# Kernel tuning notes

Measured on AMD Instinct MI355X. Metric: run time of the kernel, lower is better.

## Reference

```python
import jax, jax.numpy as jnp
import numpy as np

B, T, I, H, O = 256, 256, 16, 256, 11
HYP_HID = 512
BLD = 8
N1 = H * I + H * H + 2 * H        # RNN cell params (W_ih, W_hh, b_ih, b_hh)
N2 = O * H + O                    # readout params (W_out, b_out)


def setup_inputs() -> dict:
    key = jax.random.key(0)
    k = jax.random.split(key, 4)
    bld = jax.random.normal(k[0], (B, BLD), dtype=jnp.float32)
    stimulus = jax.random.normal(k[1], (B, T, I), dtype=jnp.float32)
    # hypnet MLP: bld -> relu -> flat per-sample params; small init to keep tanh unsaturated
    W1 = jax.random.normal(k[2], (BLD, HYP_HID), dtype=jnp.float32) * 0.05
    b1 = jnp.zeros((HYP_HID,), dtype=jnp.float32)
    W2 = jax.random.normal(k[3], (HYP_HID, N1 + N2), dtype=jnp.float32) * 0.02
    b2 = jnp.zeros((N1 + N2,), dtype=jnp.float32)
    return {"bld": bld, "stimulus": stimulus, "W1": W1, "b1": b1, "W2": W2, "b2": b2}


def reference(bld, stimulus, W1, b1, W2, b2):
    # hypernetwork: per-sample flat params [B, N1+N2]
    flat = jax.nn.relu(bld @ W1 + b1) @ W2 + b2
    params1, params2 = flat[:, :N1], flat[:, N1:]

    # unpack per-sample RNN cell params
    o = 0
    W_ih = params1[:, o:o + H * I].reshape(B, H, I); o += H * I
    W_hh = params1[:, o:o + H * H].reshape(B, H, H); o += H * H
    b_ih = params1[:, o:o + H]; o += H
    b_hh = params1[:, o:o + H]
    W_out = params2[:, :O * H].reshape(B, O, H)
    b_out = params2[:, O * H:].reshape(B, O)

    # shift stimulus right by one step with a zero frame (teacher forcing input)
    rnn_input = jnp.concatenate(
        [jnp.zeros((B, 1, I), dtype=stimulus.dtype), stimulus[:, :-1]], axis=1)

    # precompute input projection for all steps: [B, T, H]
    x_proj = jnp.einsum('bti,bhi->bth', rnn_input, W_ih) + b_ih[:, None, :]

    def step(h, xp_t):  # h: [B, H], xp_t: [B, H]
        h_next = jnp.tanh(xp_t + jnp.einsum('bh,bgh->bg', h, W_hh) + b_hh)
        return h_next, h_next

    h0 = jnp.zeros((B, H), dtype=stimulus.dtype)
    h_last, out_tm = jax.lax.scan(step, h0, jnp.swapaxes(x_proj, 0, 1))
    output1 = jnp.swapaxes(out_tm, 0, 1)  # [B, T, H]

    # per-sample linear readout [B, T, O]
    output2 = jnp.einsum('bth,boh->bto', output1, W_out) + b_out[:, None, :]
    output2 = jnp.nan_to_num(output2, nan=0.0)

    output_act = jax.nn.sigmoid(output2[:, :, :3])
    output_bldi = output2[:, :, 3:]
    h = h_last[None]  # [1, B, H]
    return (output_act, output_bldi, h, params1, params2)
```

## Files before the change

kernel.cpp:

```cpp
#include <hip/hip_runtime.h>

typedef unsigned short u16;
typedef unsigned int u32;
using short8   = __attribute__((ext_vector_type(8))) short;
using floatx4  = __attribute__((ext_vector_type(4))) float;
using half_t   = _Float16;
using half2_t  = __attribute__((ext_vector_type(2))) _Float16;
using halfx8   = __attribute__((ext_vector_type(8))) _Float16;

constexpr int B_ = 256, T_ = 256, I_ = 16, H_ = 256, O_ = 11;
constexpr int HYP = 512;
constexpr int N1_ = H_ * I_ + H_ * H_ + 2 * H_;
constexpr int N2_ = O_ * H_ + O_;
constexpr int GN  = N1_ + N2_;

constexpr size_t OUT_ACT  = 0;
constexpr size_t OUT_BLDI = (size_t)B_ * T_ * 3;
constexpr size_t OUT_H    = OUT_BLDI + (size_t)B_ * T_ * 8;
constexpr size_t OUT_P1   = OUT_H + (size_t)B_ * H_;
constexpr size_t OUT_P2   = OUT_P1 + (size_t)B_ * N1_;

__device__ inline void bar_lds() {
    asm volatile("s_waitcnt lgkmcnt(0)\n\ts_barrier" ::: "memory");
}

__device__ inline float bf2f(u16 u) {
    union { u32 i; float f; } v; v.i = ((u32)u) << 16; return v.f;
}
__device__ inline u16 f2bf(float f) {
    u32 x = __float_as_uint(f);
    u32 r = (x + 0x7fffu + ((x >> 16) & 1u)) >> 16;
    return (u16)r;
}

__device__ inline bool sniff_f32(const void* p) {
    const u16* w = (const u16*)p;
    const int lane = threadIdx.x & 63;
    u16 u = w[lane * 2];
    unsigned e = (u >> 7) & 0xFF;
    bool inband = (u == 0) || (e >= 77 && e <= 140);
    return __popcll(__ballot(inband)) < 56;
}

__device__ inline float ldr(const void* p, size_t i, bool f32) {
    return f32 ? ((const float*)p)[i] : bf2f(((const u16*)p)[i]);
}

__global__ void h1_kernel(const void* __restrict__ bld, const void* __restrict__ W1,
                          const void* __restrict__ b1, u16* __restrict__ h1) {
    const bool bldf = sniff_f32(bld);
    const bool w1f  = sniff_f32(W1);
    const bool b1f  = sniff_f32(b1);
    const int b = blockIdx.x;
    const int j = threadIdx.x;
    float acc = ldr(b1, j, b1f);
#pragma unroll
    for (int k = 0; k < 8; k++)
        acc += ldr(bld, b * 8 + k, bldf) * ldr(W1, k * HYP + j, w1f);
    h1[b * HYP + j] = f2bf(fmaxf(acc, 0.f));
}

constexpr int KS_ = 32;
constexpr int NST = HYP / KS_;
constexpr int TKP = 40;

template<bool W2F32>
__device__ void gemm_body(const u16* __restrict__ A, const void* __restrict__ Bm,
                          const void* __restrict__ b2, bool b2f,
                          float* __restrict__ out) {
    __shared__ alignas(16) u16 tileT[64][TKP];

    const int nb   = blockIdx.x * 64;
    const int tid  = threadIdx.x;
    const int lane = tid & 63;
    const int wid  = tid >> 6;
    const int l15  = lane & 15;
    const int q    = lane >> 4;

    int  col[4]; bool cv[4];
#pragma unroll
    for (int j = 0; j < 4; j++) {
        int c = nb + j * 16 + l15;
        cv[j]  = (c < GN);
        col[j] = cv[j] ? c : (GN - 1);
    }

    const u16* ap[4];
#pragma unroll
    for (int i = 0; i < 4; i++)
        ap[i] = A + (wid * 64 + i * 16 + l15) * HYP + q * 8;

    const int scol_i = tid & 63;
    const int kq     = tid >> 6;
    int gc = nb + scol_i;
    if (gc >= GN) gc = GN - 1;
    const size_t colOff = (size_t)gc;

    float pf[8]; u16 pb[8];
    {
#pragma unroll
        for (int e = 0; e < 8; e++) {
            const size_t ro = (size_t)(kq * 8 + e) * (size_t)GN + colOff;
            if constexpr (W2F32) pf[e] = ((const float*)Bm)[ro];
            else                 pb[e] = ((const u16*)Bm)[ro];
        }
    }

    floatx4 acc[4][4] = {};

    for (int ks = 0; ks < NST; ks++) {
        short8 wv8;
#pragma unroll
        for (int e = 0; e < 8; e++) {
            if constexpr (W2F32) wv8[e] = (short)f2bf(pf[e]);
            else                 wv8[e] = (short)pb[e];
        }
        *(short8*)&tileT[scol_i][kq * 8] = wv8;

        if (ks + 1 < NST) {
#pragma unroll
            for (int e = 0; e < 8; e++) {
                const size_t ro = (size_t)((ks + 1) * KS_ + kq * 8 + e) * (size_t)GN + colOff;
                if constexpr (W2F32) pf[e] = ((const float*)Bm)[ro];
                else                 pb[e] = ((const u16*)Bm)[ro];
            }
        }
        bar_lds();

        short8 af[4];
#pragma unroll
        for (int i = 0; i < 4; i++)
            af[i] = *(const short8*)(ap[i] + ks * KS_);

        short8 bfr[4];
#pragma unroll
        for (int j = 0; j < 4; j++)
            bfr[j] = *(const short8*)&tileT[j * 16 + l15][q * 8];

#pragma unroll
        for (int i = 0; i < 4; i++)
#pragma unroll
            for (int j = 0; j < 4; j++)
                acc[i][j] = __builtin_amdgcn_mfma_f32_16x16x32_bf16(af[i], bfr[j], acc[i][j], 0, 0, 0);
        bar_lds();
    }

    const bool isP2 = (nb >= N1_);
#pragma unroll
    for (int j = 0; j < 4; j++) {
        const float bias = ldr(b2, col[j], b2f);
#pragma unroll
        for (int i = 0; i < 4; i++) {
            const int mbase = wid * 64 + i * 16 + q * 4;
#pragma unroll
            for (int r = 0; r < 4; r++) {
                if (cv[j]) {
                    const float v = acc[i][j][r] + bias;
                    const int m = mbase + r;
                    size_t dst;
                    if (isP2) dst = OUT_P2 + (size_t)m * N2_ + (size_t)(col[j] - N1_);
                    else      dst = OUT_P1 + (size_t)m * N1_ + (size_t)col[j];
                    out[dst] = v;
                }
            }
        }
    }
}
__global__ __launch_bounds__(256) void gemm_kernel(const u16* A, const void* Bm,
                                                   const void* b2, float* out) {
    const bool w2f = sniff_f32(Bm);
    const bool b2f = sniff_f32(b2);
    if (w2f) gemm_body<true>(A, Bm, b2, b2f, out);
    else     gemm_body<false>(A, Bm, b2, b2f, out);
}

constexpr int HROW = 256;
constexpr int XROW = 40;

__global__ __launch_bounds__(256, 1) void rnn_kernel(const void* __restrict__ stim,
                                                     float* __restrict__ out) {
    const bool stf = sniff_f32(stim);
    const int b    = blockIdx.x;
    const int tid  = threadIdx.x;
    const int lane = tid & 63;
    const int wv   = tid >> 6;
    const int l15  = lane & 15;
    const int q    = lane >> 4;

    const float* p1 = out + OUT_P1 + (size_t)b * N1_;
    const float* p2 = out + OUT_P2 + (size_t)b * N2_;

    __shared__ alignas(16) half_t hist[(T_ + 1) * HROW];
    __shared__ alignas(16) half_t stim_s[T_ * XROW];

    if (stf) {
        const float2* sp = (const float2*)stim + (size_t)b * T_ * 8;
        for (int idx = tid; idx < (T_ - 1) * 8; idx += 256) {
            const int tt = idx >> 3, pr = idx & 7;
            float2 v = sp[idx];
            half2_t h; h.x = (half_t)v.x; h.y = (half_t)v.y;
            *(half2_t*)&stim_s[(tt + 1) * XROW + pr * 2] = h;
        }
    } else {
        const u32* sp = (const u32*)((const u16*)stim + (size_t)b * T_ * I_);
        for (int idx = tid; idx < (T_ - 1) * 8; idx += 256) {
            const int tt = idx >> 3, pr = idx & 7;
            u32 u = sp[idx];
            union { u32 i; float f; } lo2, hi2;
            lo2.i = u << 16; hi2.i = u & 0xffff0000u;
            half2_t h; h.x = (half_t)lo2.f; h.y = (half_t)hi2.f;
            *(half2_t*)&stim_s[(tt + 1) * XROW + pr * 2] = h;
        }
    }
    {
        u32* ss = (u32*)stim_s;
        const int base = tid * (XROW / 2);
        ss[base + 8] = 0x00003C00u;
#pragma unroll
        for (int z = 9; z < XROW / 2; z++) ss[base + z] = 0u;
        if (tid < 8)   ss[tid] = 0u;
        if (tid < 128) ((u32*)hist)[tid] = 0u;
    }

    halfx8 Wf[4][9];
    {
        const float* WH  = p1 + H_ * I_;
        const float* BIH = p1 + H_ * I_ + H_ * H_;
#pragma unroll
        for (int i = 0; i < 4; i++) {
            const int rr = 64 * wv + i * 16 + l15;
#pragma unroll
            for (int kt = 0; kt < 8; kt++) {
                const float4* wp = (const float4*)(WH + (size_t)rr * H_ + kt * 32 + q * 8);
                float4 r0 = wp[0], r1 = wp[1];
                halfx8 f;
                f[0] = (half_t)r0.x; f[1] = (half_t)r0.y; f[2] = (half_t)r0.z; f[3] = (half_t)r0.w;
                f[4] = (half_t)r1.x; f[5] = (half_t)r1.y; f[6] = (half_t)r1.z; f[7] = (half_t)r1.w;
                Wf[i][kt] = f;
            }
            halfx8 fx;
#pragma unroll
            for (int j = 0; j < 8; j++) fx[j] = (half_t)0.f;
            if (q < 2) {
                const float4* ip = (const float4*)(p1 + (size_t)rr * I_ + q * 8);
                float4 r0 = ip[0], r1 = ip[1];
                fx[0] = (half_t)r0.x; fx[1] = (half_t)r0.y; fx[2] = (half_t)r0.z; fx[3] = (half_t)r0.w;
                fx[4] = (half_t)r1.x; fx[5] = (half_t)r1.y; fx[6] = (half_t)r1.z; fx[7] = (half_t)r1.w;
            } else if (q == 2) {
                fx[0] = (half_t)(BIH[rr] + BIH[H_ + rr]);
            }
            Wf[i][8] = fx;
        }
    }
    __syncthreads();

    for (int t = 0; t < T_; t++) {
        halfx8 af[9];
        const half_t* hr = hist + (size_t)t * HROW + q * 8;
#pragma unroll
        for (int kt = 0; kt < 8; kt++)
            af[kt] = *(const halfx8*)(hr + kt * 32);
        af[8] = *(const halfx8*)(stim_s + (size_t)t * XROW + q * 8);

        floatx4 acc[4] = {};
#pragma unroll
        for (int kt = 0; kt < 9; kt++)
#pragma unroll
            for (int i = 0; i < 4; i++)
                acc[i] = __builtin_amdgcn_mfma_f32_16x16x32_f16(af[kt], Wf[i][kt], acc[i], 0, 0, 0);

        half_t* hw = hist + (size_t)(t + 1) * HROW;
#pragma unroll
        for (int i = 0; i < 4; i++) {
            const float s  = acc[i][0];
            const float e  = __expf(2.f * s);
            const float hn = 1.f - 2.f / (e + 1.f);
            if (lane < 16) {
                hw[64 * wv + i * 16 + l15] = (half_t)hn;
                if (t == T_ - 1) out[OUT_H + (size_t)b * H_ + 64 * wv + i * 16 + l15] = hn;
            }
        }
        bar_lds();
    }

    halfx8 Wo[8];
    float bo = 0.f;
    {
#pragma unroll
        for (int kt = 0; kt < 8; kt++) {
            halfx8 f;
#pragma unroll
            for (int j = 0; j < 8; j++) f[j] = (half_t)0.f;
            if (l15 < O_) {
                const float* wp = p2 + (size_t)l15 * H_ + kt * 32 + q * 8;
#pragma unroll
                for (int j = 0; j < 8; j++) f[j] = (half_t)wp[j];
            }
            Wo[kt] = f;
        }
        if (l15 < O_) bo = p2[O_ * H_ + l15];
    }

#pragma unroll
    for (int m = 0; m < 4; m++) {
        const int tb = (4 * wv + m) * 16;
        const half_t* hr = hist + (size_t)(tb + l15 + 1) * HROW + q * 8;
        floatx4 acc = {};
#pragma unroll
        for (int kt = 0; kt < 8; kt++) {
            halfx8 a = *(const halfx8*)(hr + kt * 32);
            acc = __builtin_amdgcn_mfma_f32_16x16x32_f16(a, Wo[kt], acc, 0, 0, 0);
        }
        if (l15 < O_) {
            const int o = l15;
#pragma unroll
            for (int r = 0; r < 4; r++) {
                const int tt = tb + q * 4 + r;
                float v2 = acc[r] + bo;
                if (o < 3) out[OUT_ACT + (size_t)b * T_ * 3 + (size_t)tt * 3 + o] = 1.f / (1.f + __expf(-v2));
                else       out[OUT_BLDI + (size_t)b * T_ * 8 + (size_t)tt * 8 + (o - 3)] = v2;
            }
        }
    }
}

extern "C" void kernel_launch(void* const* d_in, const int* in_sizes, int n_in,
                              void* d_out, int out_size, void* d_ws, size_t ws_size,
                              hipStream_t stream) {
    (void)in_sizes; (void)n_in; (void)out_size; (void)d_ws; (void)ws_size;
    const void* bld  = d_in[0];
    const void* stim = d_in[1];
    const void* W1   = d_in[2];
    const void* b1   = d_in[3];
    const void* W2   = d_in[4];
    const void* b2   = d_in[5];
    float* out = (float*)d_out;
    u16* h1 = (u16*)out;

    h1_kernel<<<B_, HYP, 0, stream>>>(bld, W1, b1, h1);
    gemm_kernel<<<(GN + 63) / 64, 256, 0, stream>>>(h1, W2, b2, out);
    rnn_kernel<<<B_, 256, 0, stream>>>(stim, out);
}
```

Before: 452.8 us.

## Double-buffer hypernet GEMM tiles and split RNN recurrence across eight waves

The hypernetwork GEMM now uses a double-buffered LDS tile with register prefetch two K-steps ahead, so only one barrier is needed per step instead of two and global loads overlap the MFMAs. The RNN kernel launches 512 threads per sample instead of 256, so each wave computes 32 hidden units per step instead of 64. This halves the serial MFMA chain on the critical path of the 256-step recurrence. The cost is more waves synchronizing at every step's barrier, and the GEMM uses more registers from the full unroll and extra prefetch buffers.

```diff
diff --git a/kernel.cpp b/kernel.cpp
--- a/kernel.cpp
+++ b/kernel.cpp
@@ -68,7 +68,7 @@
 __device__ void gemm_body(const u16* __restrict__ A, const void* __restrict__ Bm,
                           const void* __restrict__ b2, bool b2f,
                           float* __restrict__ out) {
-    __shared__ alignas(16) u16 tileT[64][TKP];
+    __shared__ alignas(16) u16 tileT[2][64][TKP];
 
     const int nb   = blockIdx.x * 64;
     const int tid  = threadIdx.x;
@@ -96,53 +96,85 @@
     if (gc >= GN) gc = GN - 1;
     const size_t colOff = (size_t)gc;
 
-    float pf[8]; u16 pb[8];
+    float pfw[8]; u16 pbw[8];
+    short8 afc[4];
+
     {
+        float t0[8]; u16 t1[8];
 #pragma unroll
         for (int e = 0; e < 8; e++) {
             const size_t ro = (size_t)(kq * 8 + e) * (size_t)GN + colOff;
-            if constexpr (W2F32) pf[e] = ((const float*)Bm)[ro];
-            else                 pb[e] = ((const u16*)Bm)[ro];
-        }
-    }
+            if constexpr (W2F32) t0[e] = ((const float*)Bm)[ro];
+            else                 t1[e] = ((const u16*)Bm)[ro];
+        }
+        short8 wv8;
+#pragma unroll
+        for (int e = 0; e < 8; e++) {
+            if constexpr (W2F32) wv8[e] = (short)f2bf(t0[e]);
+            else                 wv8[e] = (short)t1[e];
+        }
+        *(short8*)&tileT[0][scol_i][kq * 8] = wv8;
+    }
+#pragma unroll
+    for (int e = 0; e < 8; e++) {
+        const size_t ro = (size_t)(KS_ + kq * 8 + e) * (size_t)GN + colOff;
+        if constexpr (W2F32) pfw[e] = ((const float*)Bm)[ro];
+        else                 pbw[e] = ((const u16*)Bm)[ro];
+    }
+#pragma unroll
+    for (int i = 0; i < 4; i++) afc[i] = *(const short8*)(ap[i]);
+    bar_lds();
 
     floatx4 acc[4][4] = {};
 
+#pragma unroll
     for (int ks = 0; ks < NST; ks++) {
-        short8 wv8;
+        const int cur = ks & 1;
+
+        short8 bfr[4];
+#pragma unroll
+        for (int j = 0; j < 4; j++)
+            bfr[j] = *(const short8*)&tileT[cur][j * 16 + l15][q * 8];
+
+        short8 afn[4];
+        if (ks + 1 < NST) {
+#pragma unroll
+            for (int i = 0; i < 4; i++)
+                afn[i] = *(const short8*)(ap[i] + (ks + 1) * KS_);
+        }
+        float pfn[8]; u16 pbn[8];
+        if (ks + 2 < NST) {
+#pragma unroll
+            for (int e = 0; e < 8; e++) {
+                const size_t ro = (size_t)((ks + 2) * KS_ + kq * 8 + e) * (size_t)GN + colOff;
+                if constexpr (W2F32) pfn[e] = ((const float*)Bm)[ro];
+                else                 pbn[e] = ((const u16*)Bm)[ro];
+            }
+        }
+        if (ks + 1 < NST) {
+            short8 wv8;
+#pragma unroll
+            for (int e = 0; e < 8; e++) {
+                if constexpr (W2F32) wv8[e] = (short)f2bf(pfw[e]);
+                else                 wv8[e] = (short)pbw[e];
+            }
+            *(short8*)&tileT[cur ^ 1][scol_i][kq * 8] = wv8;
+        }
+
+#pragma unroll
+        for (int i = 0; i < 4; i++)
+#pragma unroll
+            for (int j = 0; j < 4; j++)
+                acc[i][j] = __builtin_amdgcn_mfma_f32_16x16x32_bf16(afc[i], bfr[j], acc[i][j], 0, 0, 0);
+        bar_lds();
+
+#pragma unroll
+        for (int i = 0; i < 4; i++) afc[i] = afn[i];
 #pragma unroll
         for (int e = 0; e < 8; e++) {
-            if constexpr (W2F32) wv8[e] = (short)f2bf(pf[e]);
-            else                 wv8[e] = (short)pb[e];
-        }
-        *(short8*)&tileT[scol_i][kq * 8] = wv8;
-
-        if (ks + 1 < NST) {
-#pragma unroll
-            for (int e = 0; e < 8; e++) {
-                const size_t ro = (size_t)((ks + 1) * KS_ + kq * 8 + e) * (size_t)GN + colOff;
-                if constexpr (W2F32) pf[e] = ((const float*)Bm)[ro];
-                else                 pb[e] = ((const u16*)Bm)[ro];
-            }
-        }
-        bar_lds();
-
-        short8 af[4];
-#pragma unroll
-        for (int i = 0; i < 4; i++)
-            af[i] = *(const short8*)(ap[i] + ks * KS_);
-
-        short8 bfr[4];
-#pragma unroll
-        for (int j = 0; j < 4; j++)
-            bfr[j] = *(const short8*)&tileT[j * 16 + l15][q * 8];
-
-#pragma unroll
-        for (int i = 0; i < 4; i++)
-#pragma unroll
-            for (int j = 0; j < 4; j++)
-                acc[i][j] = __builtin_amdgcn_mfma_f32_16x16x32_bf16(af[i], bfr[j], acc[i][j], 0, 0, 0);
-        bar_lds();
+            if constexpr (W2F32) pfw[e] = pfn[e];
+            else                 pbw[e] = pbn[e];
+        }
     }
 
     const bool isP2 = (nb >= N1_);
@@ -177,7 +209,7 @@
 constexpr int HROW = 256;
 constexpr int XROW = 40;
 
-__global__ __launch_bounds__(256, 1) void rnn_kernel(const void* __restrict__ stim,
+__global__ __launch_bounds__(512, 1) void rnn_kernel(const void* __restrict__ stim,
                                                      float* __restrict__ out) {
     const bool stf = sniff_f32(stim);
     const int b    = blockIdx.x;
@@ -195,7 +227,7 @@
 
     if (stf) {
         const float2* sp = (const float2*)stim + (size_t)b * T_ * 8;
-        for (int idx = tid; idx < (T_ - 1) * 8; idx += 256) {
+        for (int idx = tid; idx < (T_ - 1) * 8; idx += 512) {
             const int tt = idx >> 3, pr = idx & 7;
             float2 v = sp[idx];
             half2_t h; h.x = (half_t)v.x; h.y = (half_t)v.y;
@@ -203,7 +235,7 @@
         }
     } else {
         const u32* sp = (const u32*)((const u16*)stim + (size_t)b * T_ * I_);
-        for (int idx = tid; idx < (T_ - 1) * 8; idx += 256) {
+        for (int idx = tid; idx < (T_ - 1) * 8; idx += 512) {
             const int tt = idx >> 3, pr = idx & 7;
             u32 u = sp[idx];
             union { u32 i; float f; } lo2, hi2;
@@ -214,21 +246,23 @@
     }
     {
         u32* ss = (u32*)stim_s;
-        const int base = tid * (XROW / 2);
-        ss[base + 8] = 0x00003C00u;
-#pragma unroll
-        for (int z = 9; z < XROW / 2; z++) ss[base + z] = 0u;
+        if (tid < 256) {
+            const int base = tid * (XROW / 2);
+            ss[base + 8] = 0x00003C00u;
+#pragma unroll
+            for (int z = 9; z < XROW / 2; z++) ss[base + z] = 0u;
+        }
         if (tid < 8)   ss[tid] = 0u;
         if (tid < 128) ((u32*)hist)[tid] = 0u;
     }
 
-    halfx8 Wf[4][9];
+    halfx8 Wf[2][9];
     {
         const float* WH  = p1 + H_ * I_;
         const float* BIH = p1 + H_ * I_ + H_ * H_;
 #pragma unroll
-        for (int i = 0; i < 4; i++) {
-            const int rr = 64 * wv + i * 16 + l15;
+        for (int it = 0; it < 2; it++) {
+            const int rr = 32 * wv + it * 16 + l15;
 #pragma unroll
             for (int kt = 0; kt < 8; kt++) {
                 const float4* wp = (const float4*)(WH + (size_t)rr * H_ + kt * 32 + q * 8);
@@ -236,7 +270,7 @@
                 halfx8 f;
                 f[0] = (half_t)r0.x; f[1] = (half_t)r0.y; f[2] = (half_t)r0.z; f[3] = (half_t)r0.w;
                 f[4] = (half_t)r1.x; f[5] = (half_t)r1.y; f[6] = (half_t)r1.z; f[7] = (half_t)r1.w;
-                Wf[i][kt] = f;
+                Wf[it][kt] = f;
             }
             halfx8 fx;
 #pragma unroll
@@ -249,7 +283,7 @@
             } else if (q == 2) {
                 fx[0] = (half_t)(BIH[rr] + BIH[H_ + rr]);
             }
-            Wf[i][8] = fx;
+            Wf[it][8] = fx;
         }
     }
     __syncthreads();
@@ -262,22 +296,22 @@
             af[kt] = *(const halfx8*)(hr + kt * 32);
         af[8] = *(const halfx8*)(stim_s + (size_t)t * XROW + q * 8);
 
-        floatx4 acc[4] = {};
-#pragma unroll
-        for (int kt = 0; kt < 9; kt++)
-#pragma unroll
-            for (int i = 0; i < 4; i++)
-                acc[i] = __builtin_amdgcn_mfma_f32_16x16x32_f16(af[kt], Wf[i][kt], acc[i], 0, 0, 0);
+        floatx4 acc[2] = {};
+#pragma unroll
+        for (int kt = 0; kt < 9; kt++) {
+            acc[0] = __builtin_amdgcn_mfma_f32_16x16x32_f16(af[kt], Wf[0][kt], acc[0], 0, 0, 0);
+            acc[1] = __builtin_amdgcn_mfma_f32_16x16x32_f16(af[kt], Wf[1][kt], acc[1], 0, 0, 0);
+        }
 
         half_t* hw = hist + (size_t)(t + 1) * HROW;
 #pragma unroll
-        for (int i = 0; i < 4; i++) {
-            const float s  = acc[i][0];
+        for (int it = 0; it < 2; it++) {
+            const float s  = acc[it][0];
             const float e  = __expf(2.f * s);
             const float hn = 1.f - 2.f / (e + 1.f);
             if (lane < 16) {
-                hw[64 * wv + i * 16 + l15] = (half_t)hn;
-                if (t == T_ - 1) out[OUT_H + (size_t)b * H_ + 64 * wv + i * 16 + l15] = hn;
+                hw[32 * wv + it * 16 + l15] = (half_t)hn;
+                if (t == T_ - 1) out[OUT_H + (size_t)b * H_ + 32 * wv + it * 16 + l15] = hn;
             }
         }
         bar_lds();
@@ -302,8 +336,8 @@
     }
 
 #pragma unroll
-    for (int m = 0; m < 4; m++) {
-        const int tb = (4 * wv + m) * 16;
+    for (int m = 0; m < 2; m++) {
+        const int tb = (2 * wv + m) * 16;
         const half_t* hr = hist + (size_t)(tb + l15 + 1) * HROW + q * 8;
         floatx4 acc = {};
 #pragma unroll
@@ -339,5 +373,5 @@
 
     h1_kernel<<<B_, HYP, 0, stream>>>(bld, W1, b1, h1);
     gemm_kernel<<<(GN + 63) / 64, 256, 0, stream>>>(h1, W2, b2, out);
-    rnn_kernel<<<B_, 256, 0, stream>>>(stim, out);
-}
+    rnn_kernel<<<B_, 512, 0, stream>>>(stim, out);
+}
```

New measurement: 437.7 us. 3.3% less time.
